# Kernel tuning notes

Measured on AMD Instinct MI355X. Metric: run time of the kernel, lower is better.

## Reference

```python
import jax, jax.numpy as jnp
import numpy as np

LN_EPS = 1e-5

def layer_norm(x, gamma, beta):
    mu = jnp.mean(x, axis=-1, keepdims=True)
    var = jnp.mean(jnp.square(x - mu), axis=-1, keepdims=True)
    return (x - mu) * jax.lax.rsqrt(var + LN_EPS) * gamma + beta

def setup_inputs() -> dict:
    key = jax.random.key(0)
    ks = jax.random.split(key, 16)
    B, S, E, D, H, F = 4, 2048, 768, 768, 12, 3072
    dh = D // H
    sc = lambda fan_in: 1.0 / np.sqrt(fan_in)
    x = jax.random.normal(ks[0], (B, S, E), dtype=jnp.float32)
    mask = jax.random.randint(ks[1], (B, S, S), 0, 2) > 0
    # per-head projection weights, torch Linear layout [out, in]
    Wq = jax.random.uniform(ks[2], (H, dh, E), minval=-sc(E), maxval=sc(E))
    bq = jax.random.uniform(ks[3], (H, dh), minval=-sc(E), maxval=sc(E))
    Wk = jax.random.uniform(ks[4], (H, dh, E), minval=-sc(E), maxval=sc(E))
    bk = jax.random.uniform(ks[5], (H, dh), minval=-sc(E), maxval=sc(E))
    Wv = jax.random.uniform(ks[6], (H, dh, E), minval=-sc(E), maxval=sc(E))
    bv = jax.random.uniform(ks[7], (H, dh), minval=-sc(E), maxval=sc(E))
    gamma = jnp.ones((D,), dtype=jnp.float32)
    beta = jnp.zeros((D,), dtype=jnp.float32)
    W1 = jax.random.uniform(ks[8], (F, D), minval=-sc(D), maxval=sc(D))
    b1 = jax.random.uniform(ks[9], (F,), minval=-sc(D), maxval=sc(D))
    W2 = jax.random.uniform(ks[10], (D, F), minval=-sc(F), maxval=sc(F))
    b2 = jax.random.uniform(ks[11], (D,), minval=-sc(F), maxval=sc(F))
    return {"x": x, "mask": mask, "Wq": Wq, "bq": bq, "Wk": Wk, "bk": bk,
            "Wv": Wv, "bv": bv, "gamma": gamma, "beta": beta,
            "W1": W1, "b1": b1, "W2": W2, "b2": b2}

def reference(x, mask, Wq, bq, Wk, bk, Wv, bv, gamma, beta, W1, b1, W2, b2):
    B, S, E = x.shape
    # per-head projections, vectorized over heads: [B,H,S,dh]
    q = jnp.einsum('bse,hde->bhsd', x, Wq) + bq[None, :, None, :]
    k = jnp.einsum('bse,hde->bhsd', x, Wk) + bk[None, :, None, :]
    v = jnp.einsum('bse,hde->bhsd', x, Wv) + bv[None, :, None, :]
    # NOTE: original scales by len(q[0])**0.5 == sqrt(seq_len), not sqrt(d_head)
    scores = jnp.einsum('bhsd,bhtd->bhst', q, k) / jnp.sqrt(jnp.asarray(S, x.dtype))
    scores = jnp.where(mask[:, None, :, :], jnp.asarray(-1000.0, x.dtype), scores)
    # NOTE: original softmax is over dim=1 of [B,Sq,Sk] => the QUERY axis (axis 2 here)
    attn = jax.nn.softmax(scores, axis=2)
    o = jnp.einsum('bhst,bhtd->bhsd', attn, v)  # [B,H,S,dh]
    a = jnp.transpose(o, (0, 2, 1, 3)).reshape(B, S, -1)  # concat heads -> [B,S,D]
    a = layer_norm(a, gamma, beta) + a
    h = jax.nn.relu(jnp.einsum('bsd,fd->bsf', a, W1) + b1)
    b = jnp.einsum('bsf,df->bsd', h, W2) + b2
    b = layer_norm(b, gamma, beta) + b
    return b
```

## Files before the change

kernel.cpp:

```cpp
#include <hip/hip_runtime.h>
#include <hip/hip_bf16.h>
#include <stdint.h>

using bf16 = __hip_bfloat16;
typedef __attribute__((ext_vector_type(8))) short short8;
typedef __attribute__((ext_vector_type(4))) short short4v;
typedef __attribute__((ext_vector_type(4))) float f32x4;

#define MFMA16(a, b, c) __builtin_amdgcn_mfma_f32_16x16x32_bf16((a), (b), (c), 0, 0, 0)

static constexpr float SCLE = 0.031879358f;

__device__ __forceinline__ void g2l16(const void* g, void* l) {
  __builtin_amdgcn_global_load_lds((const __attribute__((address_space(1))) void*)g,
                                   (__attribute__((address_space(3))) void*)l, 16, 0, 0);
}

__device__ __forceinline__ short8 frag(const bf16* lds, int row, int slot) {
  return *(const short8*)((const char*)lds + row * 128 + (((slot ^ (row & 7)) & 7) << 4));
}

__global__ __launch_bounds__(256) void cvt_kernel(const float* __restrict__ in,
                                                  bf16* __restrict__ out, int n8) {
  int i = blockIdx.x * 256 + threadIdx.x;
  if (i >= n8) return;
  float4 f0 = ((const float4*)in)[i * 2 + 0];
  float4 f1 = ((const float4*)in)[i * 2 + 1];
  bf16 t[8] = {__float2bfloat16(f0.x), __float2bfloat16(f0.y),
               __float2bfloat16(f0.z), __float2bfloat16(f0.w),
               __float2bfloat16(f1.x), __float2bfloat16(f1.y),
               __float2bfloat16(f1.z), __float2bfloat16(f1.w)};
  ((float4*)out)[i] = *(const float4*)t;
}

__global__ void detect_kernel(const int* __restrict__ m, int* __restrict__ flag) {
  int v = m[threadIdx.x];
  unsigned long long ok = __ballot((v == 0) || (v == 1));
  if (threadIdx.x == 0) *flag = (ok == 0xFFFFFFFFFFFFFFFFULL) ? 1 : 0;
}

__global__ __launch_bounds__(256) void pack_kernel(const void* __restrict__ maskp,
                                                   const int* __restrict__ flagp,
                                                   uint32_t* __restrict__ pm) {
  const int i = blockIdx.x * 256 + threadIdx.x;
  uint32_t nib;
  if (*flagp) {
    const int4 v = ((const int4*)maskp)[i];
    nib = (v.x != 0) | ((v.y != 0) << 1) | ((v.z != 0) << 2) | ((v.w != 0) << 3);
  } else {
    const uchar4 c = ((const uchar4*)maskp)[i];
    nib = (c.x != 0) | ((c.y != 0) << 1) | ((c.z != 0) << 2) | ((c.w != 0) << 3);
  }
  uint32_t w = nib << ((i & 7) * 4);
  w |= __shfl_xor(w, 1, 64);
  w |= __shfl_xor(w, 2, 64);
  w |= __shfl_xor(w, 4, 64);
  if ((threadIdx.x & 7) == 0) pm[i >> 3] = w;
}

template <int EPI>
__global__ __launch_bounds__(256) void gemm_bt_kernel(
    const bf16* __restrict__ A, const bf16* __restrict__ Bm, int N, int K,
    const float* __restrict__ bias0, const float* __restrict__ bias1,
    const float* __restrict__ bias2, void* __restrict__ outp) {
  __shared__ bf16 aLds[128 * 32];
  __shared__ bf16 bLds[128 * 32];
  const int tid = threadIdx.x;
  const int wave = tid >> 6, lane = tid & 63;
  const int l15 = lane & 15, l4 = lane >> 4;
  const int row0 = blockIdx.y << 7, col0 = blockIdx.x << 7;
  const int wm = (wave >> 1) << 6, wn = (wave & 1) << 6;

  f32x4 acc[4][4] = {};

  const int sr = tid >> 2;
  const int sc = (tid & 3) << 3;
  const bf16* ga = A + (size_t)(row0 + sr) * K + sc;
  const bf16* gb = Bm + (size_t)(col0 + sr) * K + sc;
  const size_t rK64 = (size_t)64 * K;
  bf16* lA = &aLds[wave * 512];
  bf16* lB = &bLds[wave * 512];

  for (int k0 = 0; k0 < K; k0 += 32) {
    g2l16(ga + k0, lA);
    g2l16(ga + k0 + rK64, lA + 2048);
    g2l16(gb + k0, lB);
    g2l16(gb + k0 + rK64, lB + 2048);
    __syncthreads();
    short8 af[4], bfr[4];
#pragma unroll
    for (int i = 0; i < 4; i++)
      af[i] = *(const short8*)&aLds[(wm + i * 16 + l15) * 32 + l4 * 8];
#pragma unroll
    for (int i = 0; i < 4; i++)
      bfr[i] = *(const short8*)&bLds[(wn + i * 16 + l15) * 32 + l4 * 8];
#pragma unroll
    for (int i = 0; i < 4; i++)
#pragma unroll
      for (int j = 0; j < 4; j++) acc[i][j] = MFMA16(af[i], bfr[j], acc[i][j]);
    __syncthreads();
  }

  if (EPI == 0) {
#pragma unroll
    for (int j = 0; j < 4; j++) {
      const int gcol = col0 + wn + j * 16 + l15;
      const int which = gcol / 768;
      const int oo = gcol - which * 768;
      const float* bs = (which == 0) ? bias0 : ((which == 1) ? bias1 : bias2);
      const float bv = bs[oo];
      const int h = oo >> 6, d = oo & 63;
      if (which < 2) {
        const float scl = (which == 0) ? SCLE : 1.0f;
        bf16* outb = (bf16*)outp + (size_t)which * 6291456;
#pragma unroll
        for (int i = 0; i < 4; i++) {
#pragma unroll
          for (int r = 0; r < 4; r++) {
            const int grow = row0 + wm + i * 16 + l4 * 4 + r;
            const int b = grow >> 11, s = grow & 2047;
            outb[((size_t)((b * 12 + h) * 2048 + s)) * 64 + d] =
                __float2bfloat16((acc[i][j][r] + bv) * scl);
          }
        }
      } else {
        bf16* vt = (bf16*)outp + (size_t)2 * 6291456;
#pragma unroll
        for (int i = 0; i < 4; i++) {
          const int grow = row0 + wm + i * 16 + l4 * 4;
          const int b = grow >> 11, s = grow & 2047;
          bf16 t4[4];
#pragma unroll
          for (int r = 0; r < 4; r++) t4[r] = __float2bfloat16(acc[i][j][r] + bv);
          *(short4v*)&vt[((size_t)((b * 12 + h) * 64 + d)) * 2048 + s] =
              *(const short4v*)t4;
        }
      }
    }
  } else if (EPI == 1) {
    bf16* outb = (bf16*)outp;
#pragma unroll
    for (int j = 0; j < 4; j++) {
      const int gcol = col0 + wn + j * 16 + l15;
      const float bv = bias0[gcol];
#pragma unroll
      for (int i = 0; i < 4; i++)
#pragma unroll
        for (int r = 0; r < 4; r++) {
          const int grow = row0 + wm + i * 16 + l4 * 4 + r;
          float v = acc[i][j][r] + bv;
          v = v > 0.f ? v : 0.f;
          outb[(size_t)grow * N + gcol] = __float2bfloat16(v);
        }
    }
  } else {
    float* outf = (float*)outp;
#pragma unroll
    for (int j = 0; j < 4; j++) {
      const int gcol = col0 + wn + j * 16 + l15;
      const float bv = bias0[gcol];
#pragma unroll
      for (int i = 0; i < 4; i++)
#pragma unroll
        for (int r = 0; r < 4; r++) {
          const int grow = row0 + wm + i * 16 + l4 * 4 + r;
          outf[(size_t)grow * N + gcol] = acc[i][j][r] + bv;
        }
    }
  }
}

__global__ __launch_bounds__(256, 3) void zsum_kernel(
    const bf16* __restrict__ Qb, const bf16* __restrict__ Kb,
    const uint32_t* __restrict__ pm, float* __restrict__ rcpZ) {
  __shared__ bf16 qLds[2][64 * 64];
  const int tid = threadIdx.x, wave = tid >> 6, lane = tid & 63;
  const int l15 = lane & 15, l4 = lane >> 4;
  const int srr = lane >> 3, sss = lane & 7;
  const int bid = blockIdx.x;
  const int swz = (bid & 7) * 96 + (bid >> 3);
  const int bh = swz >> 4, ttile = swz & 15;
  const int b = bh / 12;
  const int t0 = (ttile << 7) + (wave << 5);
  const size_t qkBase = (size_t)bh * (2048 * 64);
  const bf16* Kp = Kb + qkBase;
  const bf16* Qp = Qb + qkBase;
  const uint32_t* pmB = pm + (size_t)b * 2048 * 64;
  const int widx = t0 >> 5;

  short8 ak[2][2];
#pragma unroll
  for (int tf = 0; tf < 2; tf++)
#pragma unroll
    for (int kc = 0; kc < 2; kc++)
      ak[tf][kc] = *(const short8*)(Kp + (size_t)(t0 + tf * 16 + l15) * 64 +
                                    kc * 32 + l4 * 8);

  auto stageQ = [&](int buf, int s0) {
#pragma unroll
    for (int p = 0; p < 2; p++) {
      const int r = p * 32 + wave * 8 + srr;
      g2l16(Qp + (size_t)(s0 + r) * 64 + ((sss ^ (r & 7)) << 3),
            &qLds[buf][p * 2048 + wave * 512]);
    }
  };

  f32x4 z[2] = {};
  stageQ(0, 0);
  __syncthreads();

  for (int i = 0; i < 32; i++) {
    const int s0 = i << 6;
    if (i < 31) stageQ((i + 1) & 1, s0 + 64);
    const bf16* qb = qLds[i & 1];
    uint32_t mw[4];
#pragma unroll
    for (int sf = 0; sf < 4; sf++)
      mw[sf] = pmB[(size_t)(s0 + sf * 16 + l15) * 64 + widx];
#pragma unroll
    for (int sf = 0; sf < 4; sf++) {
      const short8 q0 = frag(qb, sf * 16 + l15, l4);
      const short8 q1 = frag(qb, sf * 16 + l15, 4 + l4);
#pragma unroll
      for (int tf = 0; tf < 2; tf++) {
        __builtin_amdgcn_s_setprio(1);
        f32x4 cc = {};
        cc = MFMA16(ak[tf][0], q0, cc);
        cc = MFMA16(ak[tf][1], q1, cc);
        __builtin_amdgcn_s_setprio(0);
        const uint32_t bits = mw[sf] >> (tf * 16 + l4 * 4);
#pragma unroll
        for (int r = 0; r < 4; r++) {
          const float e = __builtin_amdgcn_exp2f(cc[r]);
          z[tf][r] += ((bits >> r) & 1) ? 0.f : e;
        }
      }
    }
    __syncthreads();
  }

#pragma unroll
  for (int tf = 0; tf < 2; tf++)
#pragma unroll
    for (int r = 0; r < 4; r++) {
      float zz = z[tf][r];
      zz += __shfl_xor(zz, 1, 64);
      zz += __shfl_xor(zz, 2, 64);
      zz += __shfl_xor(zz, 4, 64);
      zz += __shfl_xor(zz, 8, 64);
      if (l15 == 0)
        rcpZ[(size_t)bh * 2048 + t0 + tf * 16 + l4 * 4 + r] = 1.0f / zz;
    }
}

__global__ __launch_bounds__(256) void vscale_kernel(bf16* __restrict__ Vt,
                                                     const float* __restrict__ rcpZ) {
  const int i = blockIdx.x * 256 + threadIdx.x;
  if (i >= 786432) return;
  const size_t e = (size_t)i * 8;
  const int t = (int)(e & 2047);
  const int bh = (int)(e >> 17);
  const float4 r0 = *(const float4*)(rcpZ + ((size_t)bh << 11) + t);
  const float4 r1 = *(const float4*)(rcpZ + ((size_t)bh << 11) + t + 4);
  bf16 tmp[8];
  *(short8*)tmp = *(const short8*)(Vt + e);
  const float rs[8] = {r0.x, r0.y, r0.z, r0.w, r1.x, r1.y, r1.z, r1.w};
#pragma unroll
  for (int j = 0; j < 8; j++)
    tmp[j] = __float2bfloat16(__bfloat162float(tmp[j]) * rs[j]);
  *(short8*)(Vt + e) = *(const short8*)tmp;
}

__global__ __launch_bounds__(256, 3) void attn_pv_kernel(
    const bf16* __restrict__ Qb, const bf16* __restrict__ Kb,
    const bf16* __restrict__ Vt, const uint32_t* __restrict__ pm,
    float* __restrict__ aOut) {
  __shared__ bf16 kLds[2][64 * 64];
  __shared__ bf16 vLds[2][64 * 64];
  __shared__ char pbuf[4][4096];
  const int tid = threadIdx.x, wave = tid >> 6, lane = tid & 63;
  const int l15 = lane & 15, l4 = lane >> 4;
  const int srr = lane >> 3, sss = lane & 7;
  const int bid = blockIdx.x;
  const int swz = (bid & 7) * 96 + (bid >> 3);
  const int bh = swz >> 4, stile = swz & 15;
  const int b = bh / 12, h = bh - b * 12;
  const int s0 = (stile << 7) + (wave << 5);
  const size_t qkBase = (size_t)bh * (2048 * 64);
  const bf16* Kp = Kb + qkBase;
  const bf16* Qp = Qb + qkBase;
  const bf16* Vp = Vt + (size_t)bh * 64 * 2048;
  const uint32_t* pmB = pm + (size_t)b * 2048 * 64;
  char* wb = pbuf[wave];

  auto stageKV = [&](int buf, int t0) {
#pragma unroll
    for (int p = 0; p < 2; p++) {
      const int r = p * 32 + wave * 8 + srr;
      g2l16(Kp + (size_t)(t0 + r) * 64 + ((sss ^ (r & 7)) << 3),
            &kLds[buf][p * 2048 + wave * 512]);
      g2l16(Vp + (size_t)r * 2048 + t0 + ((sss ^ (r & 7)) << 3),
            &vLds[buf][p * 2048 + wave * 512]);
    }
  };

  short8 qf[2][2];
#pragma unroll
  for (int mf = 0; mf < 2; mf++)
#pragma unroll
    for (int kc = 0; kc < 2; kc++)
      qf[mf][kc] = *(const short8*)(Qp + (size_t)(s0 + mf * 16 + l15) * 64 +
                                    kc * 32 + l4 * 8);

  f32x4 oacc[2][4] = {};
  stageKV(0, 0);
  __syncthreads();

  for (int i = 0; i < 32; i++) {
    const int t0 = i << 6;
    if (i < 31) stageKV((i + 1) & 1, t0 + 64);
    const bf16* kb = kLds[i & 1];
    const bf16* vb = vLds[i & 1];
    uint2 mw[2];
#pragma unroll
    for (int mf = 0; mf < 2; mf++)
      mw[mf] = *(const uint2*)(pmB + (size_t)(s0 + mf * 16 + l15) * 64 + (t0 >> 5));

#pragma unroll
    for (int half = 0; half < 2; half++) {
#pragma unroll
      for (int tfl = 0; tfl < 2; tfl++) {
        const int trow = (half * 2 + tfl) * 16 + l15;
        const short8 a0 = frag(kb, trow, l4);
        const short8 a1 = frag(kb, trow, 4 + l4);
#pragma unroll
        for (int mf = 0; mf < 2; mf++) {
          __builtin_amdgcn_s_setprio(1);
          f32x4 cc = {};
          cc = MFMA16(a0, qf[mf][0], cc);
          cc = MFMA16(a1, qf[mf][1], cc);
          __builtin_amdgcn_s_setprio(0);
          const uint32_t bits =
              ((half == 0) ? mw[mf].x : mw[mf].y) >> (tfl * 16 + l4 * 4);
          bf16 p4[4];
#pragma unroll
          for (int r = 0; r < 4; r++) {
            const float e = __builtin_amdgcn_exp2f(cc[r]);
            p4[r] = __float2bfloat16(((bits >> r) & 1) ? 0.f : e);
          }
          const int slot = half * 4 + tfl * 2 + (l4 >> 1);
          char* dst = wb + (mf * 16 + l15) * 128 + ((slot ^ (l15 & 7)) << 4) +
                      (l4 & 1) * 8;
          *(short4v*)dst = *(const short4v*)p4;
        }
      }
      __builtin_amdgcn_s_setprio(1);
#pragma unroll
      for (int mf = 0; mf < 2; mf++) {
        const int slot = half * 4 + l4;
        const short8 ap = *(const short8*)(wb + (mf * 16 + l15) * 128 +
                                           ((slot ^ (l15 & 7)) << 4));
#pragma unroll
        for (int nf = 0; nf < 4; nf++) {
          const short8 bv = frag(vb, nf * 16 + l15, half * 4 + l4);
          oacc[mf][nf] = MFMA16(ap, bv, oacc[mf][nf]);
        }
      }
      __builtin_amdgcn_s_setprio(0);
    }
    __syncthreads();
  }

#pragma unroll
  for (int mf = 0; mf < 2; mf++)
#pragma unroll
    for (int nf = 0; nf < 4; nf++)
#pragma unroll
      for (int r = 0; r < 4; r++) {
        const int sg = s0 + mf * 16 + l4 * 4 + r;
        const int d = nf * 16 + l15;
        aOut[((size_t)(b * 2048 + sg)) * 768 + h * 64 + d] = oacc[mf][nf][r];
      }
}

template <int OUTMODE>
__global__ __launch_bounds__(256) void ln_kernel(const float* __restrict__ in,
                                                 const float* __restrict__ gamma,
                                                 const float* __restrict__ beta,
                                                 void* __restrict__ outp) {
  const int row = blockIdx.x, tid = threadIdx.x;
  const float* x = in + (size_t)row * 768;
  float v0 = x[tid], v1 = x[tid + 256], v2 = x[tid + 512];
  float s = v0 + v1 + v2;
#pragma unroll
  for (int m = 32; m >= 1; m >>= 1) s += __shfl_xor(s, m, 64);
  __shared__ float red[4];
  if ((tid & 63) == 0) red[tid >> 6] = s;
  __syncthreads();
  s = red[0] + red[1] + red[2] + red[3];
  const float mu = s * (1.f / 768.f);
  const float d0 = v0 - mu, d1 = v1 - mu, d2 = v2 - mu;
  float q = d0 * d0 + d1 * d1 + d2 * d2;
#pragma unroll
  for (int m = 32; m >= 1; m >>= 1) q += __shfl_xor(q, m, 64);
  __syncthreads();
  if ((tid & 63) == 0) red[tid >> 6] = q;
  __syncthreads();
  q = red[0] + red[1] + red[2] + red[3];
  const float rs = rsqrtf(q * (1.f / 768.f) + 1e-5f);
  const float y0 = d0 * rs * gamma[tid] + beta[tid] + v0;
  const float y1 = d1 * rs * gamma[tid + 256] + beta[tid + 256] + v1;
  const float y2 = d2 * rs * gamma[tid + 512] + beta[tid + 512] + v2;
  if (OUTMODE == 0) {
    float* o = (float*)outp + (size_t)row * 768;
    o[tid] = y0; o[tid + 256] = y1; o[tid + 512] = y2;
  } else {
    bf16* o = (bf16*)outp + (size_t)row * 768;
    o[tid] = __float2bfloat16(y0);
    o[tid + 256] = __float2bfloat16(y1);
    o[tid + 512] = __float2bfloat16(y2);
  }
}

extern "C" void kernel_launch(void* const* d_in, const int* in_sizes, int n_in,
                              void* d_out, int out_size, void* d_ws, size_t ws_size,
                              hipStream_t stream) {
  const float* x = (const float*)d_in[0];
  const void* mask = d_in[1];
  const float* Wq = (const float*)d_in[2];
  const float* bq = (const float*)d_in[3];
  const float* Wk = (const float*)d_in[4];
  const float* bk = (const float*)d_in[5];
  const float* Wv = (const float*)d_in[6];
  const float* bv = (const float*)d_in[7];
  const float* gamma = (const float*)d_in[8];
  const float* beta = (const float*)d_in[9];
  const float* W1 = (const float*)d_in[10];
  const float* b1 = (const float*)d_in[11];
  const float* W2 = (const float*)d_in[12];
  const float* b2 = (const float*)d_in[13];
  float* out = (float*)d_out;

  char* ws = (char*)d_ws;
  size_t o = 0;
  auto al = [&](size_t n) { size_t r = o; o = (o + n + 255) & ~(size_t)255; return r; };
  const size_t Q_off = al(12582912);
  const size_t K_off = al(12582912);
  const size_t V_off = al(12582912);
  const size_t XB_off = al(12582912);
  const size_t WQKV_off = al(3538944);
  const size_t H_off = Q_off;
  const size_t W1B_off = al(4718592);
  const size_t W2B_off = al(4718592);
  const size_t RZ_off = al(393216);
  const size_t A_off = al(25165824);
  const size_t BF_off = A_off;
  const size_t A2_off = al(12582912);
  const size_t FL_off = al(256);
  const size_t PM_off = al(2097152);
  if (o > ws_size) return;

  bf16* Qb = (bf16*)(ws + Q_off);
  bf16* Kb = (bf16*)(ws + K_off);
  bf16* Vt = (bf16*)(ws + V_off);
  bf16* XB = (bf16*)(ws + XB_off);
  bf16* WQKV = (bf16*)(ws + WQKV_off);
  bf16* Hb = (bf16*)(ws + H_off);
  bf16* W1B = (bf16*)(ws + W1B_off);
  bf16* W2B = (bf16*)(ws + W2B_off);
  float* rcpZ = (float*)(ws + RZ_off);
  float* Af = (float*)(ws + A_off);
  float* Bf = (float*)(ws + BF_off);
  bf16* A2b = (bf16*)(ws + A2_off);
  int* flag = (int*)(ws + FL_off);
  uint32_t* pm = (uint32_t*)(ws + PM_off);

  cvt_kernel<<<3072, 256, 0, stream>>>(x, XB, 786432);
  cvt_kernel<<<288, 256, 0, stream>>>(Wq, WQKV, 73728);
  cvt_kernel<<<288, 256, 0, stream>>>(Wk, WQKV + 589824, 73728);
  cvt_kernel<<<288, 256, 0, stream>>>(Wv, WQKV + 2 * 589824, 73728);
  cvt_kernel<<<1152, 256, 0, stream>>>(W1, W1B, 294912);
  cvt_kernel<<<1152, 256, 0, stream>>>(W2, W2B, 294912);
  detect_kernel<<<1, 64, 0, stream>>>((const int*)mask, flag);
  pack_kernel<<<16384, 256, 0, stream>>>(mask, flag, pm);

  gemm_bt_kernel<0><<<dim3(18, 64), 256, 0, stream>>>(XB, WQKV, 2304, 768, bq, bk, bv, Qb);
  zsum_kernel<<<768, 256, 0, stream>>>(Qb, Kb, pm, rcpZ);
  vscale_kernel<<<3072, 256, 0, stream>>>(Vt, rcpZ);
  attn_pv_kernel<<<768, 256, 0, stream>>>(Qb, Kb, Vt, pm, Af);
  ln_kernel<1><<<8192, 256, 0, stream>>>(Af, gamma, beta, A2b);
  gemm_bt_kernel<1><<<dim3(24, 64), 256, 0, stream>>>(A2b, W1B, 3072, 768, b1, nullptr, nullptr, Hb);
  gemm_bt_kernel<2><<<dim3(6, 64), 256, 0, stream>>>(Hb, W2B, 768, 3072, b2, nullptr, nullptr, Bf);
  ln_kernel<0><<<8192, 256, 0, stream>>>(Bf, gamma, beta, out);
}
```

Baseline: 528.0 us.

## Double-buffer GEMMs, fuse V scaling into zsum, drop P LDS round-trip

```diff
diff --git a/kernel.cpp b/kernel.cpp
--- a/kernel.cpp
+++ b/kernel.cpp
@@ -8,6 +8,21 @@
 typedef __attribute__((ext_vector_type(4))) float f32x4;
 
 #define MFMA16(a, b, c) __builtin_amdgcn_mfma_f32_16x16x32_bf16((a), (b), (c), 0, 0, 0)
+
+#if __has_builtin(__builtin_amdgcn_mfma_f32_16x16x16bf16_1k)
+#define MFMAK16(a, b, c) __builtin_amdgcn_mfma_f32_16x16x16bf16_1k((a), (b), (c), 0, 0, 0)
+#elif __has_builtin(__builtin_amdgcn_mfma_f32_16x16x16_bf16_1k)
+#define MFMAK16(a, b, c) __builtin_amdgcn_mfma_f32_16x16x16_bf16_1k((a), (b), (c), 0, 0, 0)
+#elif __has_builtin(__builtin_amdgcn_mfma_f32_16x16x16_bf16)
+#define MFMAK16(a, b, c) __builtin_amdgcn_mfma_f32_16x16x16_bf16((a), (b), (c), 0, 0, 0)
+#else
+static __device__ __forceinline__ f32x4 mfmak16_asm(short4v a, short4v b, f32x4 c) {
+  f32x4 d;
+  asm("v_mfma_f32_16x16x16_bf16 %0, %1, %2, %3" : "=v"(d) : "v"(a), "v"(b), "v"(c));
+  return d;
+}
+#define MFMAK16(a, b, c) mfmak16_asm((a), (b), (c))
+#endif
 
 static constexpr float SCLE = 0.031879358f;
 
@@ -63,8 +78,8 @@
     const bf16* __restrict__ A, const bf16* __restrict__ Bm, int N, int K,
     const float* __restrict__ bias0, const float* __restrict__ bias1,
     const float* __restrict__ bias2, void* __restrict__ outp) {
-  __shared__ bf16 aLds[128 * 32];
-  __shared__ bf16 bLds[128 * 32];
+  __shared__ bf16 aLds[2][128 * 32];
+  __shared__ bf16 bLds[2][128 * 32];
   const int tid = threadIdx.x;
   const int wave = tid >> 6, lane = tid & 63;
   const int l15 = lane & 15, l4 = lane >> 4;
@@ -78,22 +93,28 @@
   const bf16* ga = A + (size_t)(row0 + sr) * K + sc;
   const bf16* gb = Bm + (size_t)(col0 + sr) * K + sc;
   const size_t rK64 = (size_t)64 * K;
-  bf16* lA = &aLds[wave * 512];
-  bf16* lB = &bLds[wave * 512];
-
-  for (int k0 = 0; k0 < K; k0 += 32) {
-    g2l16(ga + k0, lA);
-    g2l16(ga + k0 + rK64, lA + 2048);
-    g2l16(gb + k0, lB);
-    g2l16(gb + k0 + rK64, lB + 2048);
-    __syncthreads();
+
+  auto stage = [&](int buf, int k0) {
+    g2l16(ga + k0, &aLds[buf][wave * 512]);
+    g2l16(ga + k0 + rK64, &aLds[buf][2048 + wave * 512]);
+    g2l16(gb + k0, &bLds[buf][wave * 512]);
+    g2l16(gb + k0 + rK64, &bLds[buf][2048 + wave * 512]);
+  };
+
+  stage(0, 0);
+  __syncthreads();
+  const int NT = K >> 5;
+  for (int t = 0; t < NT; t++) {
+    if (t + 1 < NT) stage((t + 1) & 1, (t + 1) << 5);
+    const bf16* la = aLds[t & 1];
+    const bf16* lb = bLds[t & 1];
     short8 af[4], bfr[4];
 #pragma unroll
     for (int i = 0; i < 4; i++)
-      af[i] = *(const short8*)&aLds[(wm + i * 16 + l15) * 32 + l4 * 8];
+      af[i] = *(const short8*)&la[(wm + i * 16 + l15) * 32 + l4 * 8];
 #pragma unroll
     for (int i = 0; i < 4; i++)
-      bfr[i] = *(const short8*)&bLds[(wn + i * 16 + l15) * 32 + l4 * 8];
+      bfr[i] = *(const short8*)&lb[(wn + i * 16 + l15) * 32 + l4 * 8];
 #pragma unroll
     for (int i = 0; i < 4; i++)
 #pragma unroll
@@ -170,31 +191,90 @@
   }
 }
 
-__global__ __launch_bounds__(256, 3) void zsum_kernel(
+__global__ __launch_bounds__(256) void gemm_bt64_kernel(
+    const bf16* __restrict__ A, const bf16* __restrict__ Bm, int N, int K,
+    const float* __restrict__ bias0, float* __restrict__ outf) {
+  __shared__ bf16 aLds[2][64 * 32];
+  __shared__ bf16 bLds[2][128 * 32];
+  const int tid = threadIdx.x;
+  const int wave = tid >> 6, lane = tid & 63;
+  const int l15 = lane & 15, l4 = lane >> 4;
+  const int row0 = blockIdx.y << 6, col0 = blockIdx.x << 7;
+  const int wm = (wave >> 1) << 5, wn = (wave & 1) << 6;
+
+  f32x4 acc[2][4] = {};
+
+  const int sr = tid >> 2;
+  const int sc = (tid & 3) << 3;
+  const bf16* ga = A + (size_t)(row0 + sr) * K + sc;
+  const bf16* gb = Bm + (size_t)(col0 + sr) * K + sc;
+  const size_t rK64 = (size_t)64 * K;
+
+  auto stage = [&](int buf, int k0) {
+    g2l16(ga + k0, &aLds[buf][wave * 512]);
+    g2l16(gb + k0, &bLds[buf][wave * 512]);
+    g2l16(gb + k0 + rK64, &bLds[buf][2048 + wave * 512]);
+  };
+
+  stage(0, 0);
+  __syncthreads();
+  const int NT = K >> 5;
+  for (int t = 0; t < NT; t++) {
+    if (t + 1 < NT) stage((t + 1) & 1, (t + 1) << 5);
+    const bf16* la = aLds[t & 1];
+    const bf16* lb = bLds[t & 1];
+    short8 af[2], bfr[4];
+#pragma unroll
+    for (int i = 0; i < 2; i++)
+      af[i] = *(const short8*)&la[(wm + i * 16 + l15) * 32 + l4 * 8];
+#pragma unroll
+    for (int j = 0; j < 4; j++)
+      bfr[j] = *(const short8*)&lb[(wn + j * 16 + l15) * 32 + l4 * 8];
+#pragma unroll
+    for (int i = 0; i < 2; i++)
+#pragma unroll
+      for (int j = 0; j < 4; j++) acc[i][j] = MFMA16(af[i], bfr[j], acc[i][j]);
+    __syncthreads();
+  }
+
+#pragma unroll
+  for (int j = 0; j < 4; j++) {
+    const int gcol = col0 + wn + j * 16 + l15;
+    const float bv = bias0[gcol];
+#pragma unroll
+    for (int i = 0; i < 2; i++)
+#pragma unroll
+      for (int r = 0; r < 4; r++) {
+        const int grow = row0 + wm + i * 16 + l4 * 4 + r;
+        outf[(size_t)grow * N + gcol] = acc[i][j][r] + bv;
+      }
+  }
+}
+
+__global__ __launch_bounds__(256) void zsum_kernel(
     const bf16* __restrict__ Qb, const bf16* __restrict__ Kb,
-    const uint32_t* __restrict__ pm, float* __restrict__ rcpZ) {
+    const uint32_t* __restrict__ pm, bf16* __restrict__ Vt) {
   __shared__ bf16 qLds[2][64 * 64];
+  __shared__ float zbuf[64];
   const int tid = threadIdx.x, wave = tid >> 6, lane = tid & 63;
   const int l15 = lane & 15, l4 = lane >> 4;
   const int srr = lane >> 3, sss = lane & 7;
   const int bid = blockIdx.x;
-  const int swz = (bid & 7) * 96 + (bid >> 3);
-  const int bh = swz >> 4, ttile = swz & 15;
+  const int swz = (bid & 7) * 192 + (bid >> 3);
+  const int bh = swz >> 5, ttile = swz & 31;
   const int b = bh / 12;
-  const int t0 = (ttile << 7) + (wave << 5);
+  const int t0 = (ttile << 6) + (wave << 4);
   const size_t qkBase = (size_t)bh * (2048 * 64);
   const bf16* Kp = Kb + qkBase;
   const bf16* Qp = Qb + qkBase;
   const uint32_t* pmB = pm + (size_t)b * 2048 * 64;
   const int widx = t0 >> 5;
-
-  short8 ak[2][2];
-#pragma unroll
-  for (int tf = 0; tf < 2; tf++)
-#pragma unroll
-    for (int kc = 0; kc < 2; kc++)
-      ak[tf][kc] = *(const short8*)(Kp + (size_t)(t0 + tf * 16 + l15) * 64 +
-                                    kc * 32 + l4 * 8);
+  const int shft = (wave & 1) * 16 + l4 * 4;
+
+  short8 ak[2];
+#pragma unroll
+  for (int kc = 0; kc < 2; kc++)
+    ak[kc] = *(const short8*)(Kp + (size_t)(t0 + l15) * 64 + kc * 32 + l4 * 8);
 
   auto stageQ = [&](int buf, int s0) {
 #pragma unroll
@@ -205,7 +285,7 @@
     }
   };
 
-  f32x4 z[2] = {};
+  f32x4 z = {};
   stageQ(0, 0);
   __syncthreads();
 
@@ -221,63 +301,52 @@
     for (int sf = 0; sf < 4; sf++) {
       const short8 q0 = frag(qb, sf * 16 + l15, l4);
       const short8 q1 = frag(qb, sf * 16 + l15, 4 + l4);
-#pragma unroll
-      for (int tf = 0; tf < 2; tf++) {
-        __builtin_amdgcn_s_setprio(1);
-        f32x4 cc = {};
-        cc = MFMA16(ak[tf][0], q0, cc);
-        cc = MFMA16(ak[tf][1], q1, cc);
-        __builtin_amdgcn_s_setprio(0);
-        const uint32_t bits = mw[sf] >> (tf * 16 + l4 * 4);
-#pragma unroll
-        for (int r = 0; r < 4; r++) {
-          const float e = __builtin_amdgcn_exp2f(cc[r]);
-          z[tf][r] += ((bits >> r) & 1) ? 0.f : e;
-        }
+      __builtin_amdgcn_s_setprio(1);
+      f32x4 cc = {};
+      cc = MFMA16(ak[0], q0, cc);
+      cc = MFMA16(ak[1], q1, cc);
+      __builtin_amdgcn_s_setprio(0);
+      const uint32_t bits = mw[sf] >> shft;
+#pragma unroll
+      for (int r = 0; r < 4; r++) {
+        const float e = __builtin_amdgcn_exp2f(cc[r]);
+        z[r] += ((bits >> r) & 1) ? 0.f : e;
       }
     }
     __syncthreads();
   }
 
 #pragma unroll
-  for (int tf = 0; tf < 2; tf++)
-#pragma unroll
-    for (int r = 0; r < 4; r++) {
-      float zz = z[tf][r];
-      zz += __shfl_xor(zz, 1, 64);
-      zz += __shfl_xor(zz, 2, 64);
-      zz += __shfl_xor(zz, 4, 64);
-      zz += __shfl_xor(zz, 8, 64);
-      if (l15 == 0)
-        rcpZ[(size_t)bh * 2048 + t0 + tf * 16 + l4 * 4 + r] = 1.0f / zz;
-    }
-}
-
-__global__ __launch_bounds__(256) void vscale_kernel(bf16* __restrict__ Vt,
-                                                     const float* __restrict__ rcpZ) {
-  const int i = blockIdx.x * 256 + threadIdx.x;
-  if (i >= 786432) return;
-  const size_t e = (size_t)i * 8;
-  const int t = (int)(e & 2047);
-  const int bh = (int)(e >> 17);
-  const float4 r0 = *(const float4*)(rcpZ + ((size_t)bh << 11) + t);
-  const float4 r1 = *(const float4*)(rcpZ + ((size_t)bh << 11) + t + 4);
-  bf16 tmp[8];
-  *(short8*)tmp = *(const short8*)(Vt + e);
-  const float rs[8] = {r0.x, r0.y, r0.z, r0.w, r1.x, r1.y, r1.z, r1.w};
-#pragma unroll
-  for (int j = 0; j < 8; j++)
-    tmp[j] = __float2bfloat16(__bfloat162float(tmp[j]) * rs[j]);
-  *(short8*)(Vt + e) = *(const short8*)tmp;
-}
-
-__global__ __launch_bounds__(256, 3) void attn_pv_kernel(
+  for (int r = 0; r < 4; r++) {
+    float zz = z[r];
+    zz += __shfl_xor(zz, 1, 64);
+    zz += __shfl_xor(zz, 2, 64);
+    zz += __shfl_xor(zz, 4, 64);
+    zz += __shfl_xor(zz, 8, 64);
+    if (l15 == 0) zbuf[(wave << 4) + (l4 << 2) + r] = 1.0f / zz;
+  }
+  __syncthreads();
+
+  const int t0blk = ttile << 6;
+  const int drow = tid >> 2;
+  const int tcol = (tid & 3) << 4;
+  bf16* vp = Vt + (size_t)bh * (64 * 2048) + (size_t)drow * 2048 + t0blk + tcol;
+  bf16 v[16];
+  *(short8*)&v[0] = *(const short8*)vp;
+  *(short8*)&v[8] = *(const short8*)(vp + 8);
+#pragma unroll
+  for (int j = 0; j < 16; j++)
+    v[j] = __float2bfloat16(__bfloat162float(v[j]) * zbuf[tcol + j]);
+  *(short8*)vp = *(const short8*)&v[0];
+  *(short8*)(vp + 8) = *(const short8*)&v[8];
+}
+
+__global__ __launch_bounds__(256, 4) void attn_pv_kernel(
     const bf16* __restrict__ Qb, const bf16* __restrict__ Kb,
     const bf16* __restrict__ Vt, const uint32_t* __restrict__ pm,
     float* __restrict__ aOut) {
   __shared__ bf16 kLds[2][64 * 64];
   __shared__ bf16 vLds[2][64 * 64];
-  __shared__ char pbuf[4][4096];
   const int tid = threadIdx.x, wave = tid >> 6, lane = tid & 63;
   const int l15 = lane & 15, l4 = lane >> 4;
   const int srr = lane >> 3, sss = lane & 7;
@@ -291,7 +360,6 @@
   const bf16* Qp = Qb + qkBase;
   const bf16* Vp = Vt + (size_t)bh * 64 * 2048;
   const uint32_t* pmB = pm + (size_t)b * 2048 * 64;
-  char* wb = pbuf[wave];
 
   auto stageKV = [&](int buf, int t0) {
 #pragma unroll
@@ -327,44 +395,37 @@
       mw[mf] = *(const uint2*)(pmB + (size_t)(s0 + mf * 16 + l15) * 64 + (t0 >> 5));
 
 #pragma unroll
-    for (int half = 0; half < 2; half++) {
-#pragma unroll
-      for (int tfl = 0; tfl < 2; tfl++) {
-        const int trow = (half * 2 + tfl) * 16 + l15;
-        const short8 a0 = frag(kb, trow, l4);
-        const short8 a1 = frag(kb, trow, 4 + l4);
-#pragma unroll
-        for (int mf = 0; mf < 2; mf++) {
-          __builtin_amdgcn_s_setprio(1);
-          f32x4 cc = {};
-          cc = MFMA16(a0, qf[mf][0], cc);
-          cc = MFMA16(a1, qf[mf][1], cc);
-          __builtin_amdgcn_s_setprio(0);
-          const uint32_t bits =
-              ((half == 0) ? mw[mf].x : mw[mf].y) >> (tfl * 16 + l4 * 4);
-          bf16 p4[4];
-#pragma unroll
-          for (int r = 0; r < 4; r++) {
-            const float e = __builtin_amdgcn_exp2f(cc[r]);
-            p4[r] = __float2bfloat16(((bits >> r) & 1) ? 0.f : e);
-          }
-          const int slot = half * 4 + tfl * 2 + (l4 >> 1);
-          char* dst = wb + (mf * 16 + l15) * 128 + ((slot ^ (l15 & 7)) << 4) +
-                      (l4 & 1) * 8;
-          *(short4v*)dst = *(const short4v*)p4;
+    for (int tf = 0; tf < 4; tf++) {
+      const int trow = tf * 16 + l15;
+      const short8 a0 = frag(kb, trow, l4);
+      const short8 a1 = frag(kb, trow, 4 + l4);
+      short4v pa[2];
+#pragma unroll
+      for (int mf = 0; mf < 2; mf++) {
+        __builtin_amdgcn_s_setprio(1);
+        f32x4 cc = {};
+        cc = MFMA16(a0, qf[mf][0], cc);
+        cc = MFMA16(a1, qf[mf][1], cc);
+        __builtin_amdgcn_s_setprio(0);
+        const uint32_t bits =
+            ((tf < 2) ? mw[mf].x : mw[mf].y) >> ((tf & 1) * 16 + l4 * 4);
+        bf16 p4[4];
+#pragma unroll
+        for (int r = 0; r < 4; r++) {
+          const float e = __builtin_amdgcn_exp2f(cc[r]);
+          p4[r] = __float2bfloat16(((bits >> r) & 1) ? 0.f : e);
         }
+        pa[mf] = *(const short4v*)p4;
       }
       __builtin_amdgcn_s_setprio(1);
 #pragma unroll
-      for (int mf = 0; mf < 2; mf++) {
-        const int slot = half * 4 + l4;
-        const short8 ap = *(const short8*)(wb + (mf * 16 + l15) * 128 +
-                                           ((slot ^ (l15 & 7)) << 4));
-#pragma unroll
-        for (int nf = 0; nf < 4; nf++) {
-          const short8 bv = frag(vb, nf * 16 + l15, half * 4 + l4);
-          oacc[mf][nf] = MFMA16(ap, bv, oacc[mf][nf]);
-        }
+      for (int nf = 0; nf < 4; nf++) {
+        const int vrow = nf * 16 + l15;
+        const short4v bv = *(const short4v*)(
+            (const char*)vb + vrow * 128 +
+            ((((tf * 2 + (l4 >> 1)) ^ (vrow & 7)) & 7) << 4) + (l4 & 1) * 8);
+        oacc[0][nf] = MFMAK16(pa[0], bv, oacc[0][nf]);
+        oacc[1][nf] = MFMAK16(pa[1], bv, oacc[1][nf]);
       }
       __builtin_amdgcn_s_setprio(0);
     }
@@ -452,7 +513,6 @@
   const size_t H_off = Q_off;
   const size_t W1B_off = al(4718592);
   const size_t W2B_off = al(4718592);
-  const size_t RZ_off = al(393216);
   const size_t A_off = al(25165824);
   const size_t BF_off = A_off;
   const size_t A2_off = al(12582912);
@@ -468,7 +528,6 @@
   bf16* Hb = (bf16*)(ws + H_off);
   bf16* W1B = (bf16*)(ws + W1B_off);
   bf16* W2B = (bf16*)(ws + W2B_off);
-  float* rcpZ = (float*)(ws + RZ_off);
   float* Af = (float*)(ws + A_off);
   float* Bf = (float*)(ws + BF_off);
   bf16* A2b = (bf16*)(ws + A2_off);
@@ -485,11 +544,10 @@
   pack_kernel<<<16384, 256, 0, stream>>>(mask, flag, pm);
 
   gemm_bt_kernel<0><<<dim3(18, 64), 256, 0, stream>>>(XB, WQKV, 2304, 768, bq, bk, bv, Qb);
-  zsum_kernel<<<768, 256, 0, stream>>>(Qb, Kb, pm, rcpZ);
-  vscale_kernel<<<3072, 256, 0, stream>>>(Vt, rcpZ);
+  zsum_kernel<<<1536, 256, 0, stream>>>(Qb, Kb, pm, Vt);
   attn_pv_kernel<<<768, 256, 0, stream>>>(Qb, Kb, Vt, pm, Af);
   ln_kernel<1><<<8192, 256, 0, stream>>>(Af, gamma, beta, A2b);
   gemm_bt_kernel<1><<<dim3(24, 64), 256, 0, stream>>>(A2b, W1B, 3072, 768, b1, nullptr, nullptr, Hb);
-  gemm_bt_kernel<2><<<dim3(6, 64), 256, 0, stream>>>(Hb, W2B, 768, 3072, b2, nullptr, nullptr, Bf);
+  gemm_bt64_kernel<<<dim3(6, 128), 256, 0, stream>>>(Hb, W2B, 768, 3072, b2, Bf);
   ln_kernel<0><<<8192, 256, 0, stream>>>(Bf, gamma, beta, out);
 }
```

New measurement: 566.3 us. +7.3%, slower.
